# Optimization experiments

Measured on AMD Instinct MI355X. Metric: run time of the kernel, lower is better.

Reference implementation:

```python
import jax, jax.numpy as jnp
import numpy as np

N_NODES = 50000


def _sage_layer(h, src, dst, W_self, W_neigh, b):
    # DGL SAGEConv with 'mean' aggregator: fc_self(h) + fc_neigh(mean_{u in N(v)} h_u) + b
    msg = h[src]                                             # [E, d] gather
    agg = jax.ops.segment_sum(msg, dst, num_segments=N_NODES)  # [N, d]
    deg = jax.ops.segment_sum(jnp.ones((src.shape[0], 1), h.dtype), dst, num_segments=N_NODES)
    mean = agg / jnp.maximum(deg, 1.0)
    return h @ W_self + mean @ W_neigh + b


def _edge_mlp(h, src, dst, Wp1, bp1, Wp2, bp2):
    # MLPPredictor: score(u,v) = W2 relu(W1 [h_u ; h_v])
    z = jnp.concatenate([h[src], h[dst]], axis=-1)           # [Ep, 2*out]
    hdn = jax.nn.relu(z @ Wp1 + bp1)
    return (hdn @ Wp2 + bp2)[:, 0]                           # [Ep]


def setup_inputs() -> dict:
    key = jax.random.key(0)
    ks = jax.random.split(key, 16)
    N, E, EP = N_NODES, 160000, 100000
    d_in, d_h, d_out = 512, 256, 64

    def glorot(k, shape):
        fan = shape[0] + shape[1]
        return jax.random.normal(k, shape, jnp.float32) * jnp.sqrt(2.0 / fan)

    return {
        "x": jax.random.normal(ks[0], (N, d_in), jnp.float32),
        "edge_src": jax.random.randint(ks[1], (E,), 0, N, jnp.int32),
        "edge_dst": jax.random.randint(ks[2], (E,), 0, N, jnp.int32),
        "pos_src": jax.random.randint(ks[3], (EP,), 0, N, jnp.int32),
        "pos_dst": jax.random.randint(ks[4], (EP,), 0, N, jnp.int32),
        "neg_src": jax.random.randint(ks[5], (EP,), 0, N, jnp.int32),
        "neg_dst": jax.random.randint(ks[6], (EP,), 0, N, jnp.int32),
        "W_self1": glorot(ks[7], (d_in, d_h)),
        "W_neigh1": glorot(ks[8], (d_in, d_h)),
        "b1": jnp.zeros((d_h,), jnp.float32),
        "W_self2": glorot(ks[9], (d_h, d_out)),
        "W_neigh2": glorot(ks[10], (d_h, d_out)),
        "b2": jnp.zeros((d_out,), jnp.float32),
        "Wp1": glorot(ks[11], (2 * d_out, d_out)),
        "bp1": jnp.zeros((d_out,), jnp.float32),
        "Wp2": glorot(ks[12], (d_out, 1)),
        "bp2": jnp.zeros((1,), jnp.float32),
    }


def reference(x, edge_src, edge_dst, pos_src, pos_dst, neg_src, neg_dst,
              W_self1, W_neigh1, b1, W_self2, W_neigh2, b2, Wp1, bp1, Wp2, bp2):
    # 2-layer SAGE (512 -> 256 -> 64), relu between layers
    h = jax.nn.relu(_sage_layer(x, edge_src, edge_dst, W_self1, W_neigh1, b1))
    h = _sage_layer(h, edge_src, edge_dst, W_self2, W_neigh2, b2)
    pos_score = _edge_mlp(h, pos_src, pos_dst, Wp1, bp1, Wp2, bp2)
    neg_score = _edge_mlp(h, neg_src, neg_dst, Wp1, bp1, Wp2, bp2)
    return (pos_score, neg_score)
```

## Files before the change

kernel.cpp:

```cpp
#include <hip/hip_runtime.h>

#define NN 50000
#define NE 160000
#define NP 100000
#define DIN 512
#define DH  256
#define DO  64
#define NBLK_SCAN 196

typedef short bf16x8 __attribute__((ext_vector_type(8)));
typedef float f32x4  __attribute__((ext_vector_type(4)));

__device__ __forceinline__ float bf2f(unsigned short u) {
    return __uint_as_float(((unsigned int)u) << 16);
}
__device__ __forceinline__ unsigned short f2bf(float f) {
    unsigned int x = __float_as_uint(f);
    return (unsigned short)((x + 0x7fffu + ((x >> 16) & 1u)) >> 16);
}

__device__ __forceinline__ void gload_lds16(const void* g, void* l) {
    __builtin_amdgcn_global_load_lds(
        (const __attribute__((address_space(1))) void*)g,
        (__attribute__((address_space(3))) void*)l, 16, 0, 0);
}

__global__ __launch_bounds__(256) void deg_count(const int* __restrict__ dst, int* __restrict__ deg) {
    int e = blockIdx.x * 256 + threadIdx.x;
    if (e < NE) atomicAdd(&deg[dst[e]], 1);
}

__global__ __launch_bounds__(256) void scan_part(const int* __restrict__ deg, int* __restrict__ excl,
                                                 int* __restrict__ bsums) {
    __shared__ int sh[256];
    int i = blockIdx.x * 256 + threadIdx.x;
    int v = (i < NN) ? deg[i] : 0;
    sh[threadIdx.x] = v;
    __syncthreads();
    #pragma unroll
    for (int off = 1; off < 256; off <<= 1) {
        int t = (threadIdx.x >= off) ? sh[threadIdx.x - off] : 0;
        __syncthreads();
        sh[threadIdx.x] += t;
        __syncthreads();
    }
    if (i < NN) excl[i] = sh[threadIdx.x] - v;
    if (threadIdx.x == 255) bsums[blockIdx.x] = sh[255];
}

__global__ __launch_bounds__(256) void scan_sums(int* __restrict__ bsums, int* __restrict__ boff) {
    __shared__ int sh[256];
    int v = (threadIdx.x < NBLK_SCAN) ? bsums[threadIdx.x] : 0;
    sh[threadIdx.x] = v;
    __syncthreads();
    #pragma unroll
    for (int off = 1; off < 256; off <<= 1) {
        int t = (threadIdx.x >= off) ? sh[threadIdx.x - off] : 0;
        __syncthreads();
        sh[threadIdx.x] += t;
        __syncthreads();
    }
    boff[threadIdx.x] = sh[threadIdx.x] - v;
}

__global__ __launch_bounds__(256) void scan_add(int* __restrict__ off, const int* __restrict__ boff,
                                                int* __restrict__ cursor) {
    int i = blockIdx.x * 256 + threadIdx.x;
    if (i < NN) {
        int o = off[i] + boff[blockIdx.x];
        off[i] = o;
        cursor[i] = o;
    }
    if (i == 0) off[NN] = NE;
}

__global__ __launch_bounds__(256) void fill_csr(const int* __restrict__ src, const int* __restrict__ dst,
                                                int* __restrict__ cursor, int* __restrict__ eidx) {
    int e = blockIdx.x * 256 + threadIdx.x;
    if (e < NE) {
        int p = atomicAdd(&cursor[dst[e]], 1);
        eidx[p] = src[e];
    }
}

__global__ __launch_bounds__(256) void prep_w(const float* __restrict__ Wself, const float* __restrict__ Wneigh,
                                              unsigned short* __restrict__ Bt, int K, int Nhalf) {
    int idx = blockIdx.x * 256 + threadIdx.x;
    int N = 2 * Nhalf;
    if (idx >= N * K) return;
    int n = idx / K, k = idx - n * K;
    float v = (n < Nhalf) ? Wself[(size_t)k * Nhalf + n] : Wneigh[(size_t)k * Nhalf + (n - Nhalf)];
    Bt[idx] = f2bf(v);
}

__global__ __launch_bounds__(256) void prep_wp1(const float* __restrict__ Wp1, unsigned short* __restrict__ Wp1b) {
    int idx = blockIdx.x * 256 + threadIdx.x;
    if (idx >= 64 * 128) return;
    int n = idx >> 7, k = idx & 127;
    Wp1b[idx] = f2bf(Wp1[(size_t)k * 64 + n]);
}

__global__ __launch_bounds__(256) void gemm_f32a(
    const float* __restrict__ A, const unsigned short* __restrict__ Bt,
    unsigned short* __restrict__ Cout, int M, int N, int K)
{
    __shared__ unsigned short As[128 * 64];
    __shared__ unsigned short Bs[128 * 64];
    const int tid = threadIdx.x;
    const int w = tid >> 6, l = tid & 63;
    const int wr = (w >> 1) * 64, wc = (w & 1) * 64;

    const int nwg = gridDim.x, gx = N >> 7;
    const int q = nwg >> 3, r = nwg & 7;
    const int xcd = blockIdx.x & 7, pos = blockIdx.x >> 3;
    const int work = (xcd < r ? xcd * (q + 1) : r * (q + 1) + (xcd - r) * q) + pos;
    const int row0 = (work / gx) * 128, col0 = (work % gx) * 128;

    f32x4 acc[4][4];
    #pragma unroll
    for (int i = 0; i < 4; ++i)
        #pragma unroll
        for (int j = 0; j < 4; ++j)
            #pragma unroll
            for (int rr = 0; rr < 4; ++rr) acc[i][j][rr] = 0.0f;

    const int wave_lds_chunk = (tid & 192) * 8;

    for (int k0 = 0; k0 < K; k0 += 64) {
        __syncthreads();
        #pragma unroll
        for (int u = 0; u < 4; ++u) {
            int c = u * 256 + tid;
            int cn = c >> 3, j = c & 7;
            int js = j ^ (cn & 7);
            gload_lds16(Bt + (size_t)(col0 + cn) * K + k0 + js * 8,
                        (void*)(Bs + (u * 256) * 8 + wave_lds_chunk));
        }
        #pragma unroll
        for (int u = 0; u < 4; ++u) {
            int c = u * 256 + tid;
            int row = c >> 3, j = c & 7;
            int grow = row0 + row; if (grow >= M) grow = M - 1;
            const float* src = A + (size_t)grow * K + k0 + j * 8;
            float4 v0 = *(const float4*)src;
            float4 v1 = *(const float4*)(src + 4);
            union { bf16x8 v; unsigned short u16[8]; } pk;
            pk.u16[0] = f2bf(v0.x); pk.u16[1] = f2bf(v0.y);
            pk.u16[2] = f2bf(v0.z); pk.u16[3] = f2bf(v0.w);
            pk.u16[4] = f2bf(v1.x); pk.u16[5] = f2bf(v1.y);
            pk.u16[6] = f2bf(v1.z); pk.u16[7] = f2bf(v1.w);
            int js = j ^ (row & 7);
            *(bf16x8*)&As[row * 64 + js * 8] = pk.v;
        }
        __syncthreads();

        #pragma unroll
        for (int kk = 0; kk < 2; ++kk) {
            bf16x8 af[4], bfv[4];
            #pragma unroll
            for (int i = 0; i < 4; ++i) {
                int row = wr + i * 16 + (l & 15);
                int ch = (kk * 4 + (l >> 4)) ^ (row & 7);
                af[i] = *(const bf16x8*)&As[row * 64 + ch * 8];
            }
            #pragma unroll
            for (int j = 0; j < 4; ++j) {
                int cc = wc + j * 16 + (l & 15);
                int ch = (kk * 4 + (l >> 4)) ^ (cc & 7);
                bfv[j] = *(const bf16x8*)&Bs[cc * 64 + ch * 8];
            }
            #pragma unroll
            for (int i = 0; i < 4; ++i)
                #pragma unroll
                for (int j = 0; j < 4; ++j)
                    acc[i][j] = __builtin_amdgcn_mfma_f32_16x16x32_bf16(af[i], bfv[j], acc[i][j], 0, 0, 0);
        }
    }

    #pragma unroll
    for (int i = 0; i < 4; ++i) {
        #pragma unroll
        for (int j = 0; j < 4; ++j) {
            int r0 = row0 + wr + i * 16 + ((l >> 4) << 2);
            int c  = col0 + wc + j * 16 + (l & 15);
            #pragma unroll
            for (int rr = 0; rr < 4; ++rr) {
                if (r0 + rr < M)
                    Cout[(size_t)(r0 + rr) * N + c] = f2bf(acc[i][j][rr]);
            }
        }
    }
}

__global__ __launch_bounds__(256) void gemm_bf16(
    const unsigned short* __restrict__ A, const unsigned short* __restrict__ Bt,
    float* __restrict__ Cout, int M, int N, int K)
{
    __shared__ unsigned short As[128 * 64];
    __shared__ unsigned short Bs[128 * 64];
    const int tid = threadIdx.x;
    const int w = tid >> 6, l = tid & 63;
    const int wr = (w >> 1) * 64, wc = (w & 1) * 64;
    const int row0 = blockIdx.y * 128, col0 = blockIdx.x * 128;

    f32x4 acc[4][4];
    #pragma unroll
    for (int i = 0; i < 4; ++i)
        #pragma unroll
        for (int j = 0; j < 4; ++j)
            #pragma unroll
            for (int rr = 0; rr < 4; ++rr) acc[i][j][rr] = 0.0f;

    const int wave_lds_chunk = (tid & 192) * 8;

    for (int k0 = 0; k0 < K; k0 += 64) {
        __syncthreads();
        #pragma unroll
        for (int u = 0; u < 4; ++u) {
            int c = u * 256 + tid;
            int row = c >> 3, j = c & 7;
            int js = j ^ (row & 7);
            int grow = row0 + row; if (grow >= M) grow = M - 1;
            gload_lds16(A + (size_t)grow * K + k0 + js * 8,
                        (void*)(As + (u * 256) * 8 + wave_lds_chunk));
        }
        #pragma unroll
        for (int u = 0; u < 4; ++u) {
            int c = u * 256 + tid;
            int cn = c >> 3, j = c & 7;
            int js = j ^ (cn & 7);
            gload_lds16(Bt + (size_t)(col0 + cn) * K + k0 + js * 8,
                        (void*)(Bs + (u * 256) * 8 + wave_lds_chunk));
        }
        __syncthreads();

        #pragma unroll
        for (int kk = 0; kk < 2; ++kk) {
            bf16x8 af[4], bfv[4];
            #pragma unroll
            for (int i = 0; i < 4; ++i) {
                int row = wr + i * 16 + (l & 15);
                int ch = (kk * 4 + (l >> 4)) ^ (row & 7);
                af[i] = *(const bf16x8*)&As[row * 64 + ch * 8];
            }
            #pragma unroll
            for (int j = 0; j < 4; ++j) {
                int cc = wc + j * 16 + (l & 15);
                int ch = (kk * 4 + (l >> 4)) ^ (cc & 7);
                bfv[j] = *(const bf16x8*)&Bs[cc * 64 + ch * 8];
            }
            #pragma unroll
            for (int i = 0; i < 4; ++i)
                #pragma unroll
                for (int j = 0; j < 4; ++j)
                    acc[i][j] = __builtin_amdgcn_mfma_f32_16x16x32_bf16(af[i], bfv[j], acc[i][j], 0, 0, 0);
        }
    }

    #pragma unroll
    for (int i = 0; i < 4; ++i) {
        #pragma unroll
        for (int j = 0; j < 4; ++j) {
            int r0 = row0 + wr + i * 16 + ((l >> 4) << 2);
            int c  = col0 + wc + j * 16 + (l & 15);
            #pragma unroll
            for (int rr = 0; rr < 4; ++rr) {
                if (r0 + rr < M)
                    Cout[(size_t)(r0 + rr) * N + c] = acc[i][j][rr];
            }
        }
    }
}

__global__ __launch_bounds__(256) void agg_combine256(
    const unsigned short* __restrict__ C1, const int* __restrict__ off, const int* __restrict__ eidx,
    const float* __restrict__ b, unsigned short* __restrict__ h1b)
{
    const int wave = threadIdx.x >> 6, lane = threadIdx.x & 63;
    const int n = blockIdx.x * 4 + wave;
    if (n >= NN) return;
    const int e0 = off[n], e1 = off[n + 1];
    float acc0 = 0.f, acc1 = 0.f, acc2 = 0.f, acc3 = 0.f;
    for (int e = e0; e < e1; ++e) {
        int s = eidx[e];
        ushort4 v = *(const ushort4*)&C1[(size_t)s * 512 + 256 + lane * 4];
        acc0 += bf2f(v.x); acc1 += bf2f(v.y); acc2 += bf2f(v.z); acc3 += bf2f(v.w);
    }
    const float rd = (e1 > e0) ? 1.0f / (float)(e1 - e0) : 1.0f;
    ushort4 sv = *(const ushort4*)&C1[(size_t)n * 512 + lane * 4];
    float4 bb = ((const float4*)b)[lane];
    ushort4 o;
    o.x = f2bf(fmaxf(bf2f(sv.x) + acc0 * rd + bb.x, 0.f));
    o.y = f2bf(fmaxf(bf2f(sv.y) + acc1 * rd + bb.y, 0.f));
    o.z = f2bf(fmaxf(bf2f(sv.z) + acc2 * rd + bb.z, 0.f));
    o.w = f2bf(fmaxf(bf2f(sv.w) + acc3 * rd + bb.w, 0.f));
    *(ushort4*)&h1b[(size_t)n * 256 + lane * 4] = o;
}

__global__ __launch_bounds__(256) void agg_combine64(
    const float* __restrict__ C2, const int* __restrict__ off, const int* __restrict__ eidx,
    const float* __restrict__ b, unsigned short* __restrict__ h2b)
{
    const int wave = threadIdx.x >> 6, lane = threadIdx.x & 63;
    const int n = blockIdx.x * 4 + wave;
    if (n >= NN) return;
    const int e0 = off[n], e1 = off[n + 1];
    float acc = 0.f;
    for (int e = e0; e < e1; ++e) {
        int s = eidx[e];
        acc += C2[(size_t)s * 128 + 64 + lane];
    }
    const float rd = (e1 > e0) ? 1.0f / (float)(e1 - e0) : 1.0f;
    h2b[(size_t)n * 64 + lane] = f2bf(C2[(size_t)n * 128 + lane] + acc * rd + b[lane]);
}

__global__ __launch_bounds__(256) void edge_mlp_mfma(
    const unsigned short* __restrict__ h2b,
    const int* __restrict__ psrc, const int* __restrict__ pdst,
    const int* __restrict__ nsrc, const int* __restrict__ ndst,
    const unsigned short* __restrict__ Wp1b, const float* __restrict__ bp1,
    const float* __restrict__ Wp2, const float* __restrict__ bp2,
    float* __restrict__ out)
{
    __shared__ unsigned short z[128 * 128];
    const int tid = threadIdx.x;
    const int w = tid >> 6, l = tid & 63;
    const int e0 = blockIdx.x * 128;

    bf16x8 bfr[4][4];
    #pragma unroll
    for (int kk = 0; kk < 4; ++kk)
        #pragma unroll
        for (int j = 0; j < 4; ++j) {
            int col = j * 16 + (l & 15);
            int ch  = kk * 4 + (l >> 4);
            bfr[kk][j] = *(const bf16x8*)(Wp1b + col * 128 + ch * 8);
        }

    #pragma unroll
    for (int p = 0; p < 8; ++p) {
        int rho = p * 32 + (tid >> 3);
        int c   = tid & 7;
        int r   = rho >> 1;
        int ep  = rho & 1;
        int e   = e0 + r; if (e >= 2 * NP) e = 2 * NP - 1;
        int node = (e < NP) ? (ep ? pdst[e] : psrc[e])
                            : (ep ? ndst[e - NP] : nsrc[e - NP]);
        bf16x8 v = *(const bf16x8*)(h2b + (size_t)node * 64 + c * 8);
        int j = ep * 8 + c;
        *(bf16x8*)&z[r * 128 + ((j ^ (r & 15)) * 8)] = v;
    }
    __syncthreads();

    f32x4 acc[2][4];
    #pragma unroll
    for (int i = 0; i < 2; ++i)
        #pragma unroll
        for (int j = 0; j < 4; ++j)
            #pragma unroll
            for (int rr = 0; rr < 4; ++rr) acc[i][j][rr] = 0.0f;

    #pragma unroll
    for (int kk = 0; kk < 4; ++kk) {
        bf16x8 af[2];
        #pragma unroll
        for (int i = 0; i < 2; ++i) {
            int row = w * 32 + i * 16 + (l & 15);
            int ch  = (kk * 4 + (l >> 4)) ^ (row & 15);
            af[i] = *(const bf16x8*)&z[row * 128 + ch * 8];
        }
        #pragma unroll
        for (int i = 0; i < 2; ++i)
            #pragma unroll
            for (int j = 0; j < 4; ++j)
                acc[i][j] = __builtin_amdgcn_mfma_f32_16x16x32_bf16(af[i], bfr[kk][j], acc[i][j], 0, 0, 0);
    }

    float bp1v[4], w2v[4];
    #pragma unroll
    for (int j = 0; j < 4; ++j) {
        bp1v[j] = bp1[j * 16 + (l & 15)];
        w2v[j]  = Wp2[j * 16 + (l & 15)];
    }
    const float b2v = bp2[0];
    #pragma unroll
    for (int i = 0; i < 2; ++i) {
        #pragma unroll
        for (int rr = 0; rr < 4; ++rr) {
            float p = 0.f;
            #pragma unroll
            for (int j = 0; j < 4; ++j) {
                float h = fmaxf(acc[i][j][rr] + bp1v[j], 0.f);
                p = fmaf(h, w2v[j], p);
            }
            #pragma unroll
            for (int off = 8; off > 0; off >>= 1)
                p += __shfl_xor(p, off, 64);
            int row = w * 32 + i * 16 + ((l >> 4) << 2) + rr;
            if ((l & 15) == 0 && e0 + row < 2 * NP)
                out[e0 + row] = p + b2v;
        }
    }
}

extern "C" void kernel_launch(void* const* d_in, const int* in_sizes, int n_in,
                              void* d_out, int out_size, void* d_ws, size_t ws_size,
                              hipStream_t stream) {
    (void)in_sizes; (void)n_in; (void)out_size; (void)ws_size;
    const float* x       = (const float*)d_in[0];
    const int*   esrc    = (const int*)d_in[1];
    const int*   edst    = (const int*)d_in[2];
    const int*   psrc    = (const int*)d_in[3];
    const int*   pdst    = (const int*)d_in[4];
    const int*   nsrc    = (const int*)d_in[5];
    const int*   ndst    = (const int*)d_in[6];
    const float* Wself1  = (const float*)d_in[7];
    const float* Wneigh1 = (const float*)d_in[8];
    const float* b1      = (const float*)d_in[9];
    const float* Wself2  = (const float*)d_in[10];
    const float* Wneigh2 = (const float*)d_in[11];
    const float* b2      = (const float*)d_in[12];
    const float* Wp1     = (const float*)d_in[13];
    const float* bp1     = (const float*)d_in[14];
    const float* Wp2     = (const float*)d_in[15];
    const float* bp2     = (const float*)d_in[16];
    float* out = (float*)d_out;

    char* w = (char*)d_ws;
    int* deg_i  = (int*)w; w += 50048 * 4;
    int* off    = (int*)w; w += 50052 * 4;
    int* cursor = (int*)w; w += 50048 * 4;
    int* bsums  = (int*)w; w += 256 * 4;
    int* boff   = (int*)w; w += 256 * 4;
    int* eidx   = (int*)w; w += 160000 * 4;
    unsigned short* Bt1  = (unsigned short*)w; w += (size_t)512 * 512 * 2;
    unsigned short* Bt2  = (unsigned short*)w; w += (size_t)128 * 256 * 2;
    unsigned short* Wp1b = (unsigned short*)w; w += (size_t)64 * 128 * 2;
    unsigned short* h1b  = (unsigned short*)w; w += (size_t)NN * DH * 2;
    unsigned short* h2b  = (unsigned short*)w; w += (size_t)NN * DO * 2;
    unsigned short* C1b  = (unsigned short*)w; w += (size_t)NN * 512 * 2;
    float* C2 = (float*)C1b;

    hipMemsetAsync(deg_i, 0, 50048 * 4, stream);
    deg_count<<<(NE + 255) / 256, 256, 0, stream>>>(edst, deg_i);
    scan_part<<<NBLK_SCAN, 256, 0, stream>>>(deg_i, off, bsums);
    scan_sums<<<1, 256, 0, stream>>>(bsums, boff);
    scan_add<<<NBLK_SCAN, 256, 0, stream>>>(off, boff, cursor);
    fill_csr<<<(NE + 255) / 256, 256, 0, stream>>>(esrc, edst, cursor, eidx);

    prep_w<<<(512 * 512 + 255) / 256, 256, 0, stream>>>(Wself1, Wneigh1, Bt1, DIN, DH);
    prep_w<<<(128 * 256 + 255) / 256, 256, 0, stream>>>(Wself2, Wneigh2, Bt2, DH, DO);
    prep_wp1<<<(64 * 128 + 255) / 256, 256, 0, stream>>>(Wp1, Wp1b);

    int nwg1 = (512 / 128) * ((NN + 127) / 128);
    gemm_f32a<<<nwg1, 256, 0, stream>>>(x, Bt1, C1b, NN, 512, DIN);
    agg_combine256<<<(NN + 3) / 4, 256, 0, stream>>>(C1b, off, eidx, b1, h1b);

    dim3 g2(1, (NN + 127) / 128);
    gemm_bf16<<<g2, 256, 0, stream>>>(h1b, Bt2, C2, NN, 128, DH);
    agg_combine64<<<(NN + 3) / 4, 256, 0, stream>>>(C2, off, eidx, b2, h2b);

    edge_mlp_mfma<<<(2 * NP + 127) / 128, 256, 0, stream>>>(h2b, psrc, pdst, nsrc, ndst,
                                                            Wp1b, bp1, Wp2, bp2, out);
}
```

Measured before the change: 206.3 us.

## Prefetch A in layer-1 GEMM, fuse prep kernels, store layer-2 output as bf16

```diff
diff --git a/kernel.cpp b/kernel.cpp
--- a/kernel.cpp
+++ b/kernel.cpp
@@ -8,6 +8,12 @@
 #define DO  64
 #define NBLK_SCAN 196
 
+#define PW1_BLKS 1024
+#define PW2_BLKS 128
+#define PWP_BLKS 32
+#define ZDEG_BLKS 196
+#define PREP_BLKS (PW1_BLKS + PW2_BLKS + PWP_BLKS + ZDEG_BLKS)
+
 typedef short bf16x8 __attribute__((ext_vector_type(8)));
 typedef float f32x4  __attribute__((ext_vector_type(4)));
 
@@ -23,6 +29,42 @@
     __builtin_amdgcn_global_load_lds(
         (const __attribute__((address_space(1))) void*)g,
         (__attribute__((address_space(3))) void*)l, 16, 0, 0);
+}
+
+__global__ __launch_bounds__(256) void prep_all(
+    const float* __restrict__ Wself1, const float* __restrict__ Wneigh1, unsigned short* __restrict__ Bt1,
+    const float* __restrict__ Wself2, const float* __restrict__ Wneigh2, unsigned short* __restrict__ Bt2,
+    const float* __restrict__ Wp1, unsigned short* __restrict__ Wp1b,
+    int* __restrict__ deg_i)
+{
+    int blk = blockIdx.x;
+    if (blk < PW1_BLKS) {
+        int idx = blk * 256 + threadIdx.x;
+        int n = idx >> 9, k = idx & 511;
+        float v = (n < DH) ? Wself1[(size_t)k * DH + n] : Wneigh1[(size_t)k * DH + (n - DH)];
+        Bt1[idx] = f2bf(v);
+        return;
+    }
+    blk -= PW1_BLKS;
+    if (blk < PW2_BLKS) {
+        int idx = blk * 256 + threadIdx.x;
+        int n = idx >> 8, k = idx & 255;
+        float v = (n < DO) ? Wself2[(size_t)k * DO + n] : Wneigh2[(size_t)k * DO + (n - DO)];
+        Bt2[idx] = f2bf(v);
+        return;
+    }
+    blk -= PW2_BLKS;
+    if (blk < PWP_BLKS) {
+        int idx = blk * 256 + threadIdx.x;
+        int n = idx >> 7, k = idx & 127;
+        Wp1b[idx] = f2bf(Wp1[(size_t)k * 64 + n]);
+        return;
+    }
+    blk -= PWP_BLKS;
+    {
+        int i = blk * 256 + threadIdx.x;
+        if (i < 50048) deg_i[i] = 0;
+    }
 }
 
 __global__ __launch_bounds__(256) void deg_count(const int* __restrict__ dst, int* __restrict__ deg) {
@@ -83,24 +125,7 @@
     }
 }
 
-__global__ __launch_bounds__(256) void prep_w(const float* __restrict__ Wself, const float* __restrict__ Wneigh,
-                                              unsigned short* __restrict__ Bt, int K, int Nhalf) {
-    int idx = blockIdx.x * 256 + threadIdx.x;
-    int N = 2 * Nhalf;
-    if (idx >= N * K) return;
-    int n = idx / K, k = idx - n * K;
-    float v = (n < Nhalf) ? Wself[(size_t)k * Nhalf + n] : Wneigh[(size_t)k * Nhalf + (n - Nhalf)];
-    Bt[idx] = f2bf(v);
-}
-
-__global__ __launch_bounds__(256) void prep_wp1(const float* __restrict__ Wp1, unsigned short* __restrict__ Wp1b) {
-    int idx = blockIdx.x * 256 + threadIdx.x;
-    if (idx >= 64 * 128) return;
-    int n = idx >> 7, k = idx & 127;
-    Wp1b[idx] = f2bf(Wp1[(size_t)k * 64 + n]);
-}
-
-__global__ __launch_bounds__(256) void gemm_f32a(
+__global__ __launch_bounds__(256) void gemm_xf32(
     const float* __restrict__ A, const unsigned short* __restrict__ Bt,
     unsigned short* __restrict__ Cout, int M, int N, int K)
 {
@@ -126,6 +151,17 @@
 
     const int wave_lds_chunk = (tid & 192) * 8;
 
+    float4 pa[4][2];
+    #pragma unroll
+    for (int u = 0; u < 4; ++u) {
+        int c = u * 256 + tid;
+        int row = c >> 3, j = c & 7;
+        int grow = row0 + row; if (grow >= M) grow = M - 1;
+        const float* s = A + (size_t)grow * K + j * 8;
+        pa[u][0] = *(const float4*)s;
+        pa[u][1] = *(const float4*)(s + 4);
+    }
+
     for (int k0 = 0; k0 < K; k0 += 64) {
         __syncthreads();
         #pragma unroll
@@ -140,19 +176,27 @@
         for (int u = 0; u < 4; ++u) {
             int c = u * 256 + tid;
             int row = c >> 3, j = c & 7;
-            int grow = row0 + row; if (grow >= M) grow = M - 1;
-            const float* src = A + (size_t)grow * K + k0 + j * 8;
-            float4 v0 = *(const float4*)src;
-            float4 v1 = *(const float4*)(src + 4);
-            union { bf16x8 v; unsigned short u16[8]; } pk;
-            pk.u16[0] = f2bf(v0.x); pk.u16[1] = f2bf(v0.y);
-            pk.u16[2] = f2bf(v0.z); pk.u16[3] = f2bf(v0.w);
-            pk.u16[4] = f2bf(v1.x); pk.u16[5] = f2bf(v1.y);
-            pk.u16[6] = f2bf(v1.z); pk.u16[7] = f2bf(v1.w);
             int js = j ^ (row & 7);
+            union { bf16x8 v; unsigned int u32[4]; } pk;
+            asm("v_cvt_pk_bf16_f32 %0, %1, %2" : "=v"(pk.u32[0]) : "v"(pa[u][0].x), "v"(pa[u][0].y));
+            asm("v_cvt_pk_bf16_f32 %0, %1, %2" : "=v"(pk.u32[1]) : "v"(pa[u][0].z), "v"(pa[u][0].w));
+            asm("v_cvt_pk_bf16_f32 %0, %1, %2" : "=v"(pk.u32[2]) : "v"(pa[u][1].x), "v"(pa[u][1].y));
+            asm("v_cvt_pk_bf16_f32 %0, %1, %2" : "=v"(pk.u32[3]) : "v"(pa[u][1].z), "v"(pa[u][1].w));
             *(bf16x8*)&As[row * 64 + js * 8] = pk.v;
         }
         __syncthreads();
+
+        if (k0 + 64 < K) {
+            #pragma unroll
+            for (int u = 0; u < 4; ++u) {
+                int c = u * 256 + tid;
+                int row = c >> 3, j = c & 7;
+                int grow = row0 + row; if (grow >= M) grow = M - 1;
+                const float* s = A + (size_t)grow * K + (k0 + 64) + j * 8;
+                pa[u][0] = *(const float4*)s;
+                pa[u][1] = *(const float4*)(s + 4);
+            }
+        }
 
         #pragma unroll
         for (int kk = 0; kk < 2; ++kk) {
@@ -194,14 +238,19 @@
 
 __global__ __launch_bounds__(256) void gemm_bf16(
     const unsigned short* __restrict__ A, const unsigned short* __restrict__ Bt,
-    float* __restrict__ Cout, int M, int N, int K)
+    unsigned short* __restrict__ Cout, int M, int N, int K)
 {
     __shared__ unsigned short As[128 * 64];
     __shared__ unsigned short Bs[128 * 64];
     const int tid = threadIdx.x;
     const int w = tid >> 6, l = tid & 63;
     const int wr = (w >> 1) * 64, wc = (w & 1) * 64;
-    const int row0 = blockIdx.y * 128, col0 = blockIdx.x * 128;
+
+    const int nwg = gridDim.x, gx = N >> 7;
+    const int q = nwg >> 3, r = nwg & 7;
+    const int xcd = blockIdx.x & 7, pos = blockIdx.x >> 3;
+    const int work = (xcd < r ? xcd * (q + 1) : r * (q + 1) + (xcd - r) * q) + pos;
+    const int row0 = (work / gx) * 128, col0 = (work % gx) * 128;
 
     f32x4 acc[4][4];
     #pragma unroll
@@ -266,7 +315,7 @@
             #pragma unroll
             for (int rr = 0; rr < 4; ++rr) {
                 if (r0 + rr < M)
-                    Cout[(size_t)(r0 + rr) * N + c] = acc[i][j][rr];
+                    Cout[(size_t)(r0 + rr) * N + c] = f2bf(acc[i][j][rr]);
             }
         }
     }
@@ -298,7 +347,7 @@
 }
 
 __global__ __launch_bounds__(256) void agg_combine64(
-    const float* __restrict__ C2, const int* __restrict__ off, const int* __restrict__ eidx,
+    const unsigned short* __restrict__ C2, const int* __restrict__ off, const int* __restrict__ eidx,
     const float* __restrict__ b, unsigned short* __restrict__ h2b)
 {
     const int wave = threadIdx.x >> 6, lane = threadIdx.x & 63;
@@ -308,10 +357,10 @@
     float acc = 0.f;
     for (int e = e0; e < e1; ++e) {
         int s = eidx[e];
-        acc += C2[(size_t)s * 128 + 64 + lane];
+        acc += bf2f(C2[(size_t)s * 128 + 64 + lane]);
     }
     const float rd = (e1 > e0) ? 1.0f / (float)(e1 - e0) : 1.0f;
-    h2b[(size_t)n * 64 + lane] = f2bf(C2[(size_t)n * 128 + lane] + acc * rd + b[lane]);
+    h2b[(size_t)n * 64 + lane] = f2bf(bf2f(C2[(size_t)n * 128 + lane]) + acc * rd + b[lane]);
 }
 
 __global__ __launch_bounds__(256) void edge_mlp_mfma(
@@ -439,26 +488,24 @@
     unsigned short* h1b  = (unsigned short*)w; w += (size_t)NN * DH * 2;
     unsigned short* h2b  = (unsigned short*)w; w += (size_t)NN * DO * 2;
     unsigned short* C1b  = (unsigned short*)w; w += (size_t)NN * 512 * 2;
-    float* C2 = (float*)C1b;
-
-    hipMemsetAsync(deg_i, 0, 50048 * 4, stream);
+    unsigned short* C2b  = C1b;
+
+    prep_all<<<PREP_BLKS, 256, 0, stream>>>(Wself1, Wneigh1, Bt1,
+                                            Wself2, Wneigh2, Bt2, Wp1, Wp1b, deg_i);
+
     deg_count<<<(NE + 255) / 256, 256, 0, stream>>>(edst, deg_i);
     scan_part<<<NBLK_SCAN, 256, 0, stream>>>(deg_i, off, bsums);
     scan_sums<<<1, 256, 0, stream>>>(bsums, boff);
     scan_add<<<NBLK_SCAN, 256, 0, stream>>>(off, boff, cursor);
     fill_csr<<<(NE + 255) / 256, 256, 0, stream>>>(esrc, edst, cursor, eidx);
 
-    prep_w<<<(512 * 512 + 255) / 256, 256, 0, stream>>>(Wself1, Wneigh1, Bt1, DIN, DH);
-    prep_w<<<(128 * 256 + 255) / 256, 256, 0, stream>>>(Wself2, Wneigh2, Bt2, DH, DO);
-    prep_wp1<<<(64 * 128 + 255) / 256, 256, 0, stream>>>(Wp1, Wp1b);
-
     int nwg1 = (512 / 128) * ((NN + 127) / 128);
-    gemm_f32a<<<nwg1, 256, 0, stream>>>(x, Bt1, C1b, NN, 512, DIN);
+    gemm_xf32<<<nwg1, 256, 0, stream>>>(x, Bt1, C1b, NN, 512, DIN);
     agg_combine256<<<(NN + 3) / 4, 256, 0, stream>>>(C1b, off, eidx, b1, h1b);
 
-    dim3 g2(1, (NN + 127) / 128);
-    gemm_bf16<<<g2, 256, 0, stream>>>(h1b, Bt2, C2, NN, 128, DH);
-    agg_combine64<<<(NN + 3) / 4, 256, 0, stream>>>(C2, off, eidx, b2, h2b);
+    int nwg2 = (128 / 128) * ((NN + 127) / 128);
+    gemm_bf16<<<nwg2, 256, 0, stream>>>(h1b, Bt2, C2b, NN, 128, DH);
+    agg_combine64<<<(NN + 3) / 4, 256, 0, stream>>>(C2b, off, eidx, b2, h2b);
 
     edge_mlp_mfma<<<(2 * NP + 127) / 128, 256, 0, stream>>>(h2b, psrc, pdst, nsrc, ndst,
                                                             Wp1b, bp1, Wp2, bp2, out);
```

Measured after the change: 176.6 us. -14.4%, faster.
